# Optimization experiments

Hardware: AMD Instinct MI355X
Metric: run time of the kernel (lower is better)

## Reference

```python
import jax, jax.numpy as jnp
import numpy as np

H, Dh = 8, 64          # heads, per-head dim
FEA = H * Dh           # 512
B, T, N = 2, 128, 128
BETA = 0.3
EPS = 1e-5
SEG = T // H


def _ln(x):
    # LayerNorm over last dim, no affine params (elementwise_affine=False)
    m = jnp.mean(x, axis=-1, keepdims=True)
    v = jnp.mean((x - m) ** 2, axis=-1, keepdims=True)
    return (x - m) / jnp.sqrt(v + EPS)


def setup_inputs() -> dict:
    key = jax.random.key(0)
    ks = jax.random.split(key, 10)
    mkw = lambda k: jax.random.normal(k, (FEA, FEA), jnp.float32) * 0.02
    return {
        "x": jax.random.normal(ks[0], (B, T, N, FEA), jnp.float32),
        "te": jax.random.normal(ks[1], (B, T, N, FEA), jnp.float32),
        "Wq": mkw(ks[2]), "bq": jnp.zeros((FEA,), jnp.float32),
        "Wk": mkw(ks[3]), "bk": jnp.zeros((FEA,), jnp.float32),
        "Wv": mkw(ks[4]), "bv": jnp.zeros((FEA,), jnp.float32),
        "Wo": mkw(ks[5]), "bo": jnp.zeros((FEA,), jnp.float32),
        "W1": mkw(ks[6]), "b1": jnp.zeros((FEA,), jnp.float32),
        "W2": mkw(ks[7]), "b2": jnp.zeros((FEA,), jnp.float32),
    }


def reference(x, te, Wq, bq, Wk, bk, Wv, bv, Wo, bo, W1, b1, W2, b2):
    xt = x + te                                        # [B,T,N,F]
    q = (xt @ Wq + bq).reshape(B, T, N, H, Dh)
    k = (xt @ Wk + bk).reshape(B, T, N, H, Dh)
    v = (xt @ Wv + bv).reshape(B, T, N, H, Dh)

    # scores[b,h,n,s,t] = q_s . k_t / sqrt(d)
    scores = jnp.einsum('bsnhd,btnhd->bhnst', q, k) / np.sqrt(Dh).astype(np.float32)

    # causal mask (Mask=True): key t <= query s
    causal = jnp.tril(jnp.ones((T, T), dtype=bool))
    scores = jnp.where(causal[None, None, None], scores, -jnp.inf)

    # segment-focus reweighting (Mask2=True): head i keeps key columns
    # [i*SEG, (i+1)*SEG) (last head extends to T) at full weight, scales
    # everything else by BETA. (-inf * BETA stays -inf.)
    cols = jnp.arange(T)
    start = jnp.arange(H) * SEG
    end = jnp.where(jnp.arange(H) == H - 1, T, start + SEG)
    focus = (cols[None, :] >= start[:, None]) & (cols[None, :] < end[:, None])  # [H,T]
    scores = jnp.where(focus[None, :, None, None, :], scores, scores * BETA)

    attn = jax.nn.softmax(scores, axis=-1)
    out = jnp.einsum('bhnst,btnhd->bsnhd', attn, v).reshape(B, T, N, FEA)

    out = out @ Wo + bo
    out = _ln(out + xt)

    # FeedForward([F,F,F], res_ln=True): linear-relu-linear + residual + LN
    h = jax.nn.relu(out @ W1 + b1)
    h = h @ W2 + b2
    return _ln(h + out)
```

## Files before the change

### kernel.cpp

```cpp
#include <hip/hip_runtime.h>
#include <math.h>

typedef unsigned int uint;
typedef unsigned short ushort;

#define FEA 512
#define NH 8
#define DH 64
#define BB 2
#define TT 128
#define NN 128
#define MTOT (BB*TT*NN)
#define SEG 16
#define BETA 0.3f
#define LNEPS 1e-5f

typedef __attribute__((ext_vector_type(8))) _Float16 f16x8;
typedef __attribute__((ext_vector_type(4))) float f32x4;
typedef __attribute__((ext_vector_type(8))) short s16x8;

static __device__ __forceinline__ ushort f2h(float x) {
  _Float16 h = (_Float16)x;
  return __builtin_bit_cast(ushort, h);
}
static __device__ __forceinline__ float h2f(ushort u) {
  return (float)__builtin_bit_cast(_Float16, u);
}

__global__ __launch_bounds__(256) void add_h(const float* __restrict__ x,
                                             const float* __restrict__ te,
                                             ushort* __restrict__ xth) {
  size_t i = ((size_t)blockIdx.x * 256 + threadIdx.x) * 8;
  float4 a0 = *(const float4*)&x[i];
  float4 a1 = *(const float4*)&x[i + 4];
  float4 b0 = *(const float4*)&te[i];
  float4 b1 = *(const float4*)&te[i + 4];
  s16x8 o;
  o[0]=(short)f2h(a0.x+b0.x); o[1]=(short)f2h(a0.y+b0.y);
  o[2]=(short)f2h(a0.z+b0.z); o[3]=(short)f2h(a0.w+b0.w);
  o[4]=(short)f2h(a1.x+b1.x); o[5]=(short)f2h(a1.y+b1.y);
  o[6]=(short)f2h(a1.z+b1.z); o[7]=(short)f2h(a1.w+b1.w);
  *(s16x8*)&xth[i] = o;
}

struct W6 { const float* s[6]; };

__global__ __launch_bounds__(256) void wconv(W6 w, ushort* __restrict__ dst) {
  __shared__ float t[32][33];
  const float* W = w.s[blockIdx.z];
  ushort* WT = dst + (size_t)blockIdx.z * FEA * FEA;
  const int k0 = blockIdx.y * 32, n0 = blockIdx.x * 32;
  const int tx = threadIdx.x & 31, ty = threadIdx.x >> 5;
  #pragma unroll
  for (int i = 0; i < 4; ++i)
    t[ty + i * 8][tx] = W[(size_t)(k0 + ty + i * 8) * FEA + n0 + tx];
  __syncthreads();
  #pragma unroll
  for (int i = 0; i < 4; ++i)
    WT[(size_t)(n0 + ty + i * 8) * FEA + k0 + tx] = f2h(t[tx][ty + i * 8]);
}

struct GArgs {
  const ushort* wt[3];
  const float* bias[3];
  ushort* out[3];
};

template<int RELU, int NW, int NWG>
__global__ __launch_bounds__(256) void gemm_h(const ushort* __restrict__ A, GArgs p) {
  __shared__ ushort As[2][4096];
  __shared__ ushort Bs[2][4096];
  const int tid = threadIdx.x;
  constexpr int CPX = NWG / 8;
  constexpr int XS = (NW == 3) ? 12 : 4;
  const int wl = (blockIdx.x & 7) * CPX + (blockIdx.x >> 3);
  const int xw = wl % XS;
  const int m0 = (wl / XS) * 128;
  const int wsel = (NW == 3) ? (xw >> 2) : 0;
  const int n0 = ((NW == 3) ? (xw & 3) : xw) * 128;
  const ushort* __restrict__ WT = p.wt[wsel];
  const float*  __restrict__ bias = p.bias[wsel];
  ushort* __restrict__ C = p.out[wsel];
  const int lane = tid & 63;
  const int wid = tid >> 6;
  const int wm = wid >> 1, wn = wid & 1;
  const int c = lane & 15, g = lane >> 4;

  f32x4 acc[4][4] = {};

  int r_[2], kq_[2];
  #pragma unroll
  for (int cc = 0; cc < 2; ++cc) {
    int i = cc * 256 + tid;
    r_[cc] = i >> 2;
    kq_[cc] = (i & 3) ^ ((r_[cc] >> 1) & 3);
  }

  auto stage = [&](int buf, int k0) {
    #pragma unroll
    for (int cc = 0; cc < 2; ++cc) {
      const ushort* ga = A  + (size_t)(m0 + r_[cc]) * 512 + k0 + kq_[cc] * 8;
      const ushort* gb = WT + (size_t)(n0 + r_[cc]) * 512 + k0 + kq_[cc] * 8;
      __builtin_amdgcn_global_load_lds(
          (const __attribute__((address_space(1))) void*)ga,
          (__attribute__((address_space(3))) void*)&As[buf][(cc * 256 + tid) * 8], 16, 0, 0);
      __builtin_amdgcn_global_load_lds(
          (const __attribute__((address_space(1))) void*)gb,
          (__attribute__((address_space(3))) void*)&Bs[buf][(cc * 256 + tid) * 8], 16, 0, 0);
    }
  };

  stage(0, 0);
  __syncthreads();
  int cur = 0;
  for (int t = 0; t < 16; ++t) {
    if (t < 15) stage(cur ^ 1, (t + 1) * 32);

    f16x8 af[4], bfr[4];
    #pragma unroll
    for (int s = 0; s < 4; ++s) {
      int ra = wm * 64 + s * 16 + c;
      int sa = ra * 4 + (g ^ ((ra >> 1) & 3));
      af[s] = *(const f16x8*)&As[cur][sa * 8];
      int rb = wn * 64 + s * 16 + c;
      int sb = rb * 4 + (g ^ ((rb >> 1) & 3));
      bfr[s] = *(const f16x8*)&Bs[cur][sb * 8];
    }
    #pragma unroll
    for (int i = 0; i < 4; ++i)
      #pragma unroll
      for (int j = 0; j < 4; ++j)
        acc[i][j] = __builtin_amdgcn_mfma_f32_16x16x32_f16(bfr[j], af[i], acc[i][j], 0, 0, 0);

    __syncthreads();
    cur ^= 1;
  }

  float4 bv4[4];
  #pragma unroll
  for (int j = 0; j < 4; ++j)
    bv4[j] = *(const float4*)&bias[n0 + wn * 64 + j * 16 + g * 4];
  #pragma unroll
  for (int i = 0; i < 4; ++i) {
    const size_t rb = (size_t)(m0 + wm * 64 + i * 16 + c) * 512;
    #pragma unroll
    for (int j = 0; j < 4; ++j) {
      const int nb = n0 + wn * 64 + j * 16 + g * 4;
      float o0 = acc[i][j][0] + bv4[j].x;
      float o1 = acc[i][j][1] + bv4[j].y;
      float o2 = acc[i][j][2] + bv4[j].z;
      float o3 = acc[i][j][3] + bv4[j].w;
      if (RELU) {
        o0 = fmaxf(o0, 0.f); o1 = fmaxf(o1, 0.f);
        o2 = fmaxf(o2, 0.f); o3 = fmaxf(o3, 0.f);
      }
      uint2 pk;
      pk.x = (uint)f2h(o0) | ((uint)f2h(o1) << 16);
      pk.y = (uint)f2h(o2) | ((uint)f2h(o3) << 16);
      *(uint2*)&C[rb + nb] = pk;
    }
  }
}

__global__ __launch_bounds__(256) void attn_mfma(const ushort* __restrict__ kp,
                                                 const ushort* __restrict__ vp,
                                                 ushort* __restrict__ qo) {
  __shared__ ushort Ks[8192];
  __shared__ ushort Vt[8192];
  __shared__ ushort Pb[4][1024];
  __shared__ float  Lb[4][32];

  const int bid = blockIdx.x;
  const int h = bid & 7;
  const int n = (bid >> 3) & 127;
  const int b = bid >> 10;
  const int tid = threadIdx.x;
  const int lane = tid & 63;
  const int w = tid >> 6;
  const int g = lane >> 4, c = lane & 15;
  const size_t tstride = (size_t)NN * FEA;
  const size_t base = ((size_t)b * TT * NN + n) * FEA + (size_t)h * DH;

  #pragma unroll
  for (int it = 0; it < 4; ++it) {
    int i = it * 256 + tid;
    int t = i >> 3;
    int gd = (i & 7) ^ (t & 7);
    const ushort* gk = kp + base + (size_t)t * tstride + gd * 8;
    __builtin_amdgcn_global_load_lds(
        (const __attribute__((address_space(1))) void*)gk,
        (__attribute__((address_space(3))) void*)&Ks[i * 8], 16, 0, 0);
  }
  #pragma unroll
  for (int it = 0; it < 4; ++it) {
    int j = it * 256 + tid;
    int t = j >> 3, d0 = (j & 7) * 8;
    s16x8 vv = *(const s16x8*)&vp[base + (size_t)t * tstride + d0];
    #pragma unroll
    for (int jj = 0; jj < 8; ++jj) {
      int d = d0 + jj;
      int slot = d * 16 + ((t >> 3) ^ (d & 7) ^ (d >> 3));
      Vt[slot * 8 + (t & 7)] = (ushort)vv[jj];
    }
  }
  const int qb = w * 32;
  f16x8 Qf[2][2];
  #pragma unroll
  for (int qt = 0; qt < 2; ++qt)
    #pragma unroll
    for (int kf = 0; kf < 2; ++kf)
      Qf[qt][kf] = *(const f16x8*)
          &qo[base + (size_t)(qb + qt * 16 + c) * tstride + kf * 32 + g * 8];
  __syncthreads();

  const int fs = h * SEG;
  const int fe = (h == NH - 1) ? TT : fs + SEG;

  f32x4 Oa[2][4];
  #pragma unroll
  for (int qt = 0; qt < 2; ++qt)
    #pragma unroll
    for (int dt = 0; dt < 4; ++dt)
      Oa[qt][dt] = (f32x4){0.f, 0.f, 0.f, 0.f};
  float lsum[2] = {0.f, 0.f};

  for (int ch = 0; ch <= w; ++ch) {
    const int tc = ch * 32;
    f32x4 sf[2][2];
    #pragma unroll
    for (int tt2 = 0; tt2 < 2; ++tt2) {
      f16x8 Kf[2];
      #pragma unroll
      for (int kf = 0; kf < 2; ++kf) {
        int t = tc + tt2 * 16 + c;
        int slot = t * 8 + ((kf * 4 + g) ^ (c & 7));
        Kf[kf] = *(const f16x8*)&Ks[slot * 8];
      }
      #pragma unroll
      for (int qt = 0; qt < 2; ++qt) {
        f32x4 s = (f32x4){0.f, 0.f, 0.f, 0.f};
        s = __builtin_amdgcn_mfma_f32_16x16x32_f16(Kf[0], Qf[qt][0], s, 0, 0, 0);
        s = __builtin_amdgcn_mfma_f32_16x16x32_f16(Kf[1], Qf[qt][1], s, 0, 0, 0);
        sf[tt2][qt] = s;
      }
    }
    #pragma unroll
    for (int tt2 = 0; tt2 < 2; ++tt2) {
      #pragma unroll
      for (int qt = 0; qt < 2; ++qt) {
        const int q = qb + qt * 16 + c;
        const int qr = qt * 16 + c;
        #pragma unroll
        for (int pr = 0; pr < 2; ++pr) {
          float pv[2];
          #pragma unroll
          for (int rr = 0; rr < 2; ++rr) {
            int reg = pr * 2 + rr;
            int t = tc + tt2 * 16 + g * 4 + reg;
            float mult = (t >= fs && t < fe) ? 0.125f : 0.125f * BETA;
            float p = __expf(sf[tt2][qt][reg] * mult);
            p = (t <= q) ? p : 0.f;
            pv[rr] = p;
            lsum[qt] += p;
          }
          uint pk = (uint)f2h(pv[0]) | ((uint)f2h(pv[1]) << 16);
          int tl = tt2 * 16 + g * 4 + pr * 2;
          int slot = qr * 4 + ((tl >> 3) ^ (qr & 3));
          *(uint*)&Pb[w][slot * 8 + (tl & 7)] = pk;
        }
      }
    }
    f16x8 Vf[4];
    #pragma unroll
    for (int dt = 0; dt < 4; ++dt) {
      int d = dt * 16 + c;
      int slot = d * 16 + ((((tc >> 3)) + g) ^ (d & 7) ^ (d >> 3));
      Vf[dt] = *(const f16x8*)&Vt[slot * 8];
    }
    #pragma unroll
    for (int qt = 0; qt < 2; ++qt) {
      int qr = qt * 16 + c;
      int slot = qr * 4 + (g ^ (qr & 3));
      f16x8 Pa = *(const f16x8*)&Pb[w][slot * 8];
      #pragma unroll
      for (int dt = 0; dt < 4; ++dt)
        Oa[qt][dt] = __builtin_amdgcn_mfma_f32_16x16x32_f16(Pa, Vf[dt], Oa[qt][dt], 0, 0, 0);
    }
  }

  #pragma unroll
  for (int qt = 0; qt < 2; ++qt) {
    lsum[qt] += __shfl_xor(lsum[qt], 16, 64);
    lsum[qt] += __shfl_xor(lsum[qt], 32, 64);
  }
  if (g == 0) {
    Lb[w][c]      = 1.0f / lsum[0];
    Lb[w][16 + c] = 1.0f / lsum[1];
  }
  #pragma unroll
  for (int qt = 0; qt < 2; ++qt) {
    f32x4 linv = *(const f32x4*)&Lb[w][qt * 16 + g * 4];
    #pragma unroll
    for (int dt = 0; dt < 4; ++dt) {
      #pragma unroll
      for (int reg = 0; reg < 4; ++reg) {
        int q = qb + qt * 16 + g * 4 + reg;
        qo[base + (size_t)q * tstride + dt * 16 + c] = f2h(Oa[qt][dt][reg] * linv[reg]);
      }
    }
  }
}

template<int AH, int RH, int OH>
__global__ __launch_bounds__(256) void ln_add(const void* __restrict__ a_,
                                              const void* __restrict__ r_,
                                              void* __restrict__ y_) {
  const int lane = threadIdx.x & 63;
  const int w = threadIdx.x >> 6;
  const size_t row = (size_t)blockIdx.x * 4 + w;
  const size_t off = row * FEA + (size_t)lane * 8;
  float ua[8], ur[8], u[8];
  if (AH) {
    s16x8 v = *(const s16x8*)&((const ushort*)a_)[off];
    #pragma unroll
    for (int j = 0; j < 8; ++j) ua[j] = h2f((ushort)v[j]);
  } else {
    float4 v0 = *(const float4*)&((const float*)a_)[off];
    float4 v1 = *(const float4*)&((const float*)a_)[off + 4];
    ua[0]=v0.x; ua[1]=v0.y; ua[2]=v0.z; ua[3]=v0.w;
    ua[4]=v1.x; ua[5]=v1.y; ua[6]=v1.z; ua[7]=v1.w;
  }
  if (RH) {
    s16x8 v = *(const s16x8*)&((const ushort*)r_)[off];
    #pragma unroll
    for (int j = 0; j < 8; ++j) ur[j] = h2f((ushort)v[j]);
  } else {
    float4 v0 = *(const float4*)&((const float*)r_)[off];
    float4 v1 = *(const float4*)&((const float*)r_)[off + 4];
    ur[0]=v0.x; ur[1]=v0.y; ur[2]=v0.z; ur[3]=v0.w;
    ur[4]=v1.x; ur[5]=v1.y; ur[6]=v1.z; ur[7]=v1.w;
  }
  float sum = 0.f, sq = 0.f;
  #pragma unroll
  for (int j = 0; j < 8; ++j) {
    u[j] = ua[j] + ur[j];
    sum += u[j];
    sq = fmaf(u[j], u[j], sq);
  }
  #pragma unroll
  for (int m = 1; m < 64; m <<= 1) {
    sum += __shfl_xor(sum, m, 64);
    sq  += __shfl_xor(sq,  m, 64);
  }
  const float mean = sum * (1.0f / FEA);
  const float var = sq * (1.0f / FEA) - mean * mean;
  const float rstd = rsqrtf(var + LNEPS);
  if (OH) {
    s16x8 o;
    #pragma unroll
    for (int j = 0; j < 8; ++j) o[j] = (short)f2h((u[j] - mean) * rstd);
    *(s16x8*)&((ushort*)y_)[off] = o;
  } else {
    float4 o0, o1;
    o0.x=(u[0]-mean)*rstd; o0.y=(u[1]-mean)*rstd; o0.z=(u[2]-mean)*rstd; o0.w=(u[3]-mean)*rstd;
    o1.x=(u[4]-mean)*rstd; o1.y=(u[5]-mean)*rstd; o1.z=(u[6]-mean)*rstd; o1.w=(u[7]-mean)*rstd;
    *(float4*)&((float*)y_)[off] = o0;
    *(float4*)&((float*)y_)[off + 4] = o1;
  }
}

extern "C" void kernel_launch(void* const* d_in, const int* in_sizes, int n_in,
                              void* d_out, int out_size, void* d_ws, size_t ws_size,
                              hipStream_t stream) {
  const float* x  = (const float*)d_in[0];
  const float* te = (const float*)d_in[1];
  const float* bq = (const float*)d_in[3];
  const float* bk = (const float*)d_in[5];
  const float* bv = (const float*)d_in[7];
  const float* bo = (const float*)d_in[9];
  const float* b1 = (const float*)d_in[11];
  const float* b2 = (const float*)d_in[13];
  float* out = (float*)d_out;

  const size_t E = (size_t)MTOT * FEA;
  ushort* B0 = (ushort*)d_ws;
  ushort* B1 = B0 + E;
  ushort* B2 = B1 + E;
  ushort* B3 = B2 + E;
  ushort* WB = B3 + E;
  const size_t WE = (size_t)FEA * FEA;

  add_h<<<E / 8 / 256, 256, 0, stream>>>(x, te, B0);
  W6 w;
  w.s[0] = (const float*)d_in[2];  w.s[1] = (const float*)d_in[4];
  w.s[2] = (const float*)d_in[6];  w.s[3] = (const float*)d_in[8];
  w.s[4] = (const float*)d_in[10]; w.s[5] = (const float*)d_in[12];
  wconv<<<dim3(16, 16, 6), 256, 0, stream>>>(w, WB);
  GArgs gqkv;
  gqkv.wt[0] = WB;          gqkv.bias[0] = bq; gqkv.out[0] = B1;
  gqkv.wt[1] = WB + WE;     gqkv.bias[1] = bk; gqkv.out[1] = B2;
  gqkv.wt[2] = WB + 2 * WE; gqkv.bias[2] = bv; gqkv.out[2] = B3;
  gemm_h<0, 3, 3072><<<3072, 256, 0, stream>>>(B0, gqkv);
  attn_mfma<<<BB * NN * NH, 256, 0, stream>>>(B2, B3, B1);
  GArgs go = {};
  go.wt[0] = WB + 3 * WE; go.bias[0] = bo; go.out[0] = B2;
  gemm_h<0, 1, 1024><<<1024, 256, 0, stream>>>(B1, go);
  ln_add<1, 1, 1><<<MTOT / 4, 256, 0, stream>>>(B2, B0, B0);
  GArgs g1 = {};
  g1.wt[0] = WB + 4 * WE; g1.bias[0] = b1; g1.out[0] = B3;
  gemm_h<1, 1, 1024><<<1024, 256, 0, stream>>>(B0, g1);
  GArgs g2 = {};
  g2.wt[0] = WB + 5 * WE; g2.bias[0] = b2; g2.out[0] = B1;
  gemm_h<0, 1, 1024><<<1024, 256, 0, stream>>>(B3, g2);
  ln_add<1, 1, 0><<<MTOT / 4, 256, 0, stream>>>(B1, B0, out);
}
```

Measured before the change: 431.4 us.

## Prefetch two K-tiles ahead in GEMM with explicit waitcnt barriers

The GEMM main loop now issues loads for two stages up front and refills each buffer right after its fragments are read into registers. Explicit vmcnt/lgkmcnt waits and raw s_barrier replace __syncthreads, so global-to-LDS loads stay in flight across MFMA work instead of draining at every iteration. The add kernel also has each thread handle two 8-element chunks with half the grid, giving more loads in flight per thread. The hand-placed wait counts rely on each stage issuing exactly four loads; if that count or the ordering is wrong, the kernel can read stale LDS data.

```diff
diff --git a/kernel.cpp b/kernel.cpp
--- a/kernel.cpp
+++ b/kernel.cpp
@@ -30,17 +30,28 @@
 __global__ __launch_bounds__(256) void add_h(const float* __restrict__ x,
                                              const float* __restrict__ te,
                                              ushort* __restrict__ xth) {
-  size_t i = ((size_t)blockIdx.x * 256 + threadIdx.x) * 8;
-  float4 a0 = *(const float4*)&x[i];
-  float4 a1 = *(const float4*)&x[i + 4];
-  float4 b0 = *(const float4*)&te[i];
-  float4 b1 = *(const float4*)&te[i + 4];
-  s16x8 o;
-  o[0]=(short)f2h(a0.x+b0.x); o[1]=(short)f2h(a0.y+b0.y);
-  o[2]=(short)f2h(a0.z+b0.z); o[3]=(short)f2h(a0.w+b0.w);
-  o[4]=(short)f2h(a1.x+b1.x); o[5]=(short)f2h(a1.y+b1.y);
-  o[6]=(short)f2h(a1.z+b1.z); o[7]=(short)f2h(a1.w+b1.w);
-  *(s16x8*)&xth[i] = o;
+  const size_t half = (size_t)MTOT * FEA / 2;
+  size_t i0 = ((size_t)blockIdx.x * 256 + threadIdx.x) * 8;
+  size_t i1 = i0 + half;
+  float4 a0 = *(const float4*)&x[i0];
+  float4 a1 = *(const float4*)&x[i0 + 4];
+  float4 c0 = *(const float4*)&x[i1];
+  float4 c1 = *(const float4*)&x[i1 + 4];
+  float4 b0 = *(const float4*)&te[i0];
+  float4 b1 = *(const float4*)&te[i0 + 4];
+  float4 d0 = *(const float4*)&te[i1];
+  float4 d1 = *(const float4*)&te[i1 + 4];
+  s16x8 o0, o1;
+  o0[0]=(short)f2h(a0.x+b0.x); o0[1]=(short)f2h(a0.y+b0.y);
+  o0[2]=(short)f2h(a0.z+b0.z); o0[3]=(short)f2h(a0.w+b0.w);
+  o0[4]=(short)f2h(a1.x+b1.x); o0[5]=(short)f2h(a1.y+b1.y);
+  o0[6]=(short)f2h(a1.z+b1.z); o0[7]=(short)f2h(a1.w+b1.w);
+  o1[0]=(short)f2h(c0.x+d0.x); o1[1]=(short)f2h(c0.y+d0.y);
+  o1[2]=(short)f2h(c0.z+d0.z); o1[3]=(short)f2h(c0.w+d0.w);
+  o1[4]=(short)f2h(c1.x+d1.x); o1[5]=(short)f2h(c1.y+d1.y);
+  o1[6]=(short)f2h(c1.z+d1.z); o1[7]=(short)f2h(c1.w+d1.w);
+  *(s16x8*)&xth[i0] = o0;
+  *(s16x8*)&xth[i1] = o1;
 }
 
 struct W6 { const float* s[6]; };
@@ -111,29 +122,43 @@
   };
 
   stage(0, 0);
-  __syncthreads();
-  int cur = 0;
+  stage(1, 32);
+  asm volatile("s_waitcnt vmcnt(4)" ::: "memory");
+  __builtin_amdgcn_sched_barrier(0);
+  __builtin_amdgcn_s_barrier();
+
+  #pragma unroll
   for (int t = 0; t < 16; ++t) {
-    if (t < 15) stage(cur ^ 1, (t + 1) * 32);
+    const int bi = t & 1;
 
     f16x8 af[4], bfr[4];
     #pragma unroll
     for (int s = 0; s < 4; ++s) {
       int ra = wm * 64 + s * 16 + c;
       int sa = ra * 4 + (g ^ ((ra >> 1) & 3));
-      af[s] = *(const f16x8*)&As[cur][sa * 8];
+      af[s] = *(const f16x8*)&As[bi][sa * 8];
       int rb = wn * 64 + s * 16 + c;
       int sb = rb * 4 + (g ^ ((rb >> 1) & 3));
-      bfr[s] = *(const f16x8*)&Bs[cur][sb * 8];
-    }
+      bfr[s] = *(const f16x8*)&Bs[bi][sb * 8];
+    }
+    asm volatile("s_waitcnt lgkmcnt(0)" ::: "memory");
+    __builtin_amdgcn_sched_barrier(0);
+    __builtin_amdgcn_s_barrier();
+
+    if (t + 2 < 16) stage(bi, (t + 2) * 32);
+
     #pragma unroll
     for (int i = 0; i < 4; ++i)
       #pragma unroll
       for (int j = 0; j < 4; ++j)
         acc[i][j] = __builtin_amdgcn_mfma_f32_16x16x32_f16(bfr[j], af[i], acc[i][j], 0, 0, 0);
 
-    __syncthreads();
-    cur ^= 1;
+    if (t < 15) {
+      if (t < 14) { asm volatile("s_waitcnt vmcnt(4)" ::: "memory"); }
+      else        { asm volatile("s_waitcnt vmcnt(0)" ::: "memory"); }
+      __builtin_amdgcn_sched_barrier(0);
+      __builtin_amdgcn_s_barrier();
+    }
   }
 
   float4 bv4[4];
@@ -390,7 +415,7 @@
   ushort* WB = B3 + E;
   const size_t WE = (size_t)FEA * FEA;
 
-  add_h<<<E / 8 / 256, 256, 0, stream>>>(x, te, B0);
+  add_h<<<E / 16 / 256, 256, 0, stream>>>(x, te, B0);
   W6 w;
   w.s[0] = (const float*)d_in[2];  w.s[1] = (const float*)d_in[4];
   w.s[2] = (const float*)d_in[6];  w.s[3] = (const float*)d_in[8];
```

After: 405.8 us. -6.0%, faster.
